# Kernel tuning notes

Measured on AMD Instinct MI355X. Metric: run time of the kernel, lower is better.

Reference implementation:

```python
import jax, jax.numpy as jnp
import numpy as np

# ---- Mamba2 / model hyperparameters (from init_kwargs + mamba_ssm defaults) ----
D_MODEL = 64
D_STATE = 64
D_CONV = 4
EXPAND = 2
HEADDIM = 64                      # mamba_ssm Mamba2 default
D_INNER = EXPAND * D_MODEL        # 128
NHEADS = D_INNER // HEADDIM       # 2
CONV_DIM = D_INNER + 2 * D_STATE  # 256 (ngroups=1)
D_IN_PROJ = 2 * D_INNER + 2 * D_STATE + NHEADS  # 386
B, T, F_ = 4, 128, 128
EPS = 1e-5


def silu(x):
    return x * jax.nn.sigmoid(x)


def depthwise_causal_conv(x, w, b):
    # x: [N, L, C], w: [C, K], b: [C]  (causal depthwise conv, as in Mamba2)
    xt = x.transpose(0, 2, 1)           # [N, C, L]
    kernel = w[:, None, :]              # [C, 1, K]
    y = jax.lax.conv_general_dilated(
        xt, kernel, window_strides=(1,), padding=[(D_CONV - 1, 0)],
        feature_group_count=CONV_DIM)
    return y.transpose(0, 2, 1) + b     # [N, L, C]


def mamba2(u, Wp, cw, cb, dtb, Al, Dp, nw, Wo):
    # u: [N, L, D_MODEL]
    Nb, L, _ = u.shape
    zxbcdt = u @ Wp.T                                   # [N, L, D_IN_PROJ]
    z = zxbcdt[..., :D_INNER]
    xBC = zxbcdt[..., D_INNER:D_INNER + CONV_DIM]
    dt = jax.nn.softplus(zxbcdt[..., -NHEADS:] + dtb)   # [N, L, H]
    xBC = silu(depthwise_causal_conv(xBC, cw, cb))
    x = xBC[..., :D_INNER].reshape(Nb, L, NHEADS, HEADDIM)
    Bm = xBC[..., D_INNER:D_INNER + D_STATE]            # [N, L, Nst]
    Cm = xBC[..., D_INNER + D_STATE:]                   # [N, L, Nst]
    dA = jnp.exp(dt * (-jnp.exp(Al)))                   # [N, L, H]

    def step(h, inp):
        # h: [N, H, P, Nst]
        dA_t, dt_t, x_t, B_t, C_t = inp
        h = h * dA_t[:, :, None, None] + (dt_t[:, :, None] * x_t)[..., None] * B_t[:, None, None, :]
        y = jnp.einsum('bhpn,bn->bhp', h, C_t)
        return h, y

    h0 = jnp.zeros((Nb, NHEADS, HEADDIM, D_STATE), u.dtype)
    xs = (dA.transpose(1, 0, 2), dt.transpose(1, 0, 2),
          x.transpose(1, 0, 2, 3), Bm.transpose(1, 0, 2), Cm.transpose(1, 0, 2))
    _, ys = jax.lax.scan(step, h0, xs)                  # ys: [L, N, H, P]
    y = ys.transpose(1, 0, 2, 3) + Dp[None, None, :, None] * x
    y = y.reshape(Nb, L, D_INNER)
    # RMSNormGated (norm_before_gate=False): gate then rms-normalize
    g = y * silu(z)
    g = g * jax.lax.rsqrt(jnp.mean(g * g, axis=-1, keepdims=True) + EPS) * nw
    return g @ Wo.T                                     # [N, L, D_MODEL]


def bimamba(u, p_fwd, p_bwd, fW, fb):
    out_f = mamba2(u, *p_fwd)
    out_b = mamba2(u[:, ::-1], *p_bwd)[:, ::-1]
    return jnp.concatenate([out_f, out_b], axis=-1) @ fW.T + fb


def layernorm(x, w, b):
    m = jnp.mean(x, axis=-1, keepdims=True)
    v = jnp.mean((x - m) ** 2, axis=-1, keepdims=True)
    return (x - m) * jax.lax.rsqrt(v + EPS) * w + b


def setup_inputs() -> dict:
    key = jax.random.key(0)
    ks = jax.random.split(key, 12)
    inp = {
        'x': jax.random.normal(ks[0], (B, D_MODEL, T, F_), jnp.float32),
        # 4 Mamba2 instances stacked: [freq_fwd, freq_bwd, time_fwd, time_bwd]
        'in_proj_W': 0.02 * jax.random.normal(ks[1], (4, D_IN_PROJ, D_MODEL), jnp.float32),
        'conv_W': 0.1 * jax.random.normal(ks[2], (4, CONV_DIM, D_CONV), jnp.float32),
        'conv_b': jnp.zeros((4, CONV_DIM), jnp.float32),
        'dt_bias': 0.1 * jax.random.normal(ks[3], (4, NHEADS), jnp.float32),
        'A_log': jnp.log(jax.random.uniform(ks[4], (4, NHEADS), jnp.float32, 1.0, 16.0)),
        'D_param': 0.1 * jax.random.normal(ks[5], (4, NHEADS), jnp.float32),
        'norm_w': jnp.ones((4, D_INNER), jnp.float32),
        'out_W': 0.02 * jax.random.normal(ks[6], (4, D_MODEL, D_INNER), jnp.float32),
        # 2 BiMamba fusion linears: [freq, time]
        'fusion_W': 0.02 * jax.random.normal(ks[7], (2, D_MODEL, 2 * D_MODEL), jnp.float32),
        'fusion_b': jnp.zeros((2, D_MODEL), jnp.float32),
        # 2 LayerNorms: [freq, time]
        'ln_w': jnp.ones((2, D_MODEL), jnp.float32),
        'ln_b': jnp.zeros((2, D_MODEL), jnp.float32),
    }
    return inp


def reference(x, in_proj_W, conv_W, conv_b, dt_bias, A_log, D_param, norm_w, out_W,
              fusion_W, fusion_b, ln_w, ln_b):
    Bb, Cc, Tt, Ff = x.shape

    def mp(i):
        return (in_proj_W[i], conv_W[i], conv_b[i], dt_bias[i], A_log[i],
                D_param[i], norm_w[i], out_W[i])

    # ---- frequency axis scan (dilation == 1) ----
    x_freq = x.transpose(0, 2, 3, 1).reshape(Bb * Tt, Ff, Cc)
    xf_out = bimamba(layernorm(x_freq, ln_w[0], ln_b[0]), mp(0), mp(1), fusion_W[0], fusion_b[0])
    x = x + xf_out.reshape(Bb, Tt, Ff, Cc).transpose(0, 3, 1, 2)

    # ---- time axis scan ----
    x_time = x.transpose(0, 3, 2, 1).reshape(Bb * Ff, Tt, Cc)
    xt_out = bimamba(layernorm(x_time, ln_w[1], ln_b[1]), mp(2), mp(3), fusion_W[1], fusion_b[1])
    x = x + xt_out.reshape(Bb, Ff, Tt, Cc).transpose(0, 3, 2, 1)
    return x
```

## Files before the change

### kernel.cpp

```cpp
#include <hip/hip_runtime.h>

#define EPSV 1e-5f

typedef short bf16x8 __attribute__((ext_vector_type(8)));
typedef float f32x4 __attribute__((ext_vector_type(4)));

__device__ __forceinline__ float sigmoidf_(float x) {
  return 1.f / (1.f + __expf(-x));
}
__device__ __forceinline__ unsigned short f2bf(float f) {
  unsigned int u = __float_as_uint(f);
  u += 0x7fffu + ((u >> 16) & 1u);
  return (unsigned short)(u >> 16);
}
__device__ __forceinline__ float bfu(unsigned short h) {
  union { unsigned int u; float f; } t; t.u = ((unsigned int)h) << 16; return t.f;
}
__device__ __forceinline__ float bflo(unsigned int u) {
  union { unsigned int x; float f; } t; t.x = u << 16; return t.f;
}
__device__ __forceinline__ float bfhi(unsigned int u) {
  union { unsigned int x; float f; } t; t.x = u & 0xffff0000u; return t.f;
}

__global__ __launch_bounds__(256) void precomp_wc(
    const float* __restrict__ fW,
    const float* __restrict__ oW,
    float* __restrict__ Wc)
{
  const int bi = blockIdx.x;
  const int i = bi >> 3, mg = bi & 7;
  const int m = (mg << 3) + (threadIdx.x >> 5);
  const int k0 = (threadIdx.x & 31) << 2;
  const int p = i >> 1, d = i & 1;
  const float* fr = fW + p * 8192 + m * 128 + d * 64;
  const float* orow = oW + i * 8192 + k0;
  float a0 = 0.f, a1 = 0.f, a2 = 0.f, a3 = 0.f;
  for (int j = 0; j < 64; ++j) {
    const float f = fr[j];
    const float4 o4 = *(const float4*)(orow + j * 128);
    a0 += f * o4.x; a1 += f * o4.y; a2 += f * o4.z; a3 += f * o4.w;
  }
  float* out = Wc + i * 8192 + m * 128 + k0;
  out[0] = a0; out[1] = a1; out[2] = a2; out[3] = a3;
}

__global__ __launch_bounds__(256) void precomp_wcf(
    const float* __restrict__ Wc, unsigned short* __restrict__ WcF)
{
  const int ip = blockIdx.x;
  const float* src = Wc + (size_t)ip * 8192;
  unsigned short* dst = WcF + (size_t)ip * 8192;
  for (int idx = threadIdx.x; idx < 8192; idx += 256) {
    const int tile = idx >> 11;
    const int h = (idx >> 9) & 3;
    const int lane = (idx >> 3) & 63;
    const int j = idx & 7;
    const int col = lane & 15, quad = lane >> 4;
    dst[idx] = f2bf(src[(tile * 16 + col) * 128 + h * 32 + quad * 8 + j]);
  }
}

__global__ __launch_bounds__(256) void precomp_wpf(
    const float* __restrict__ Wp, unsigned short* __restrict__ WpF)
{
  const int ip = blockIdx.x;
  const float* src = Wp + (size_t)ip * 24704;
  unsigned short* dst = WpF + (size_t)ip * 25600;
  for (int idx = threadIdx.x; idx < 25600; idx += 256) {
    const int tile = idx >> 10;
    const int rem = idx & 1023;
    const int h = rem >> 9;
    const int lane = (rem >> 3) & 63;
    const int j = idx & 7;
    const int col = lane & 15, quad = lane >> 4;
    const int o = tile * 16 + col;
    const int k = h * 32 + quad * 8 + j;
    dst[idx] = (o < 386) ? f2bf(src[o * 64 + k]) : (unsigned short)0;
  }
}

__global__ __launch_bounds__(256) void transp0(
    const float* __restrict__ x, float* __restrict__ x0)
{
  __shared__ float T[64 * 132];
  const int tid = threadIdx.x, blk = blockIdx.x;
  const int b = blk >> 7, t = blk & 127;
  {
    const int c = tid >> 2, f0 = (tid & 3) << 5;
    const float* xp = x + (((size_t)(b * 64 + c) * 128 + t) << 7) + f0;
    float* tp = &T[c * 132 + f0];
    #pragma unroll
    for (int j = 0; j < 8; ++j)
      *(float4*)(tp + (j << 2)) = *(const float4*)(xp + (j << 2));
  }
  __syncthreads();
  {
    const int f = tid >> 1, cb = (tid & 1) << 5;
    float* op = x0 + (((size_t)(b * 128 + t) * 128 + f) << 6) + cb;
    #pragma unroll
    for (int j = 0; j < 32; j += 4) {
      float4 v;
      v.x = T[(cb + j + 0) * 132 + f];
      v.y = T[(cb + j + 1) * 132 + f];
      v.z = T[(cb + j + 2) * 132 + f];
      v.w = T[(cb + j + 3) * 132 + f];
      *(float4*)(op + j) = v;
    }
  }
}

__global__ __launch_bounds__(512, 4) void mamba_dir(
    const float* __restrict__ src,
    unsigned short* __restrict__ ybuf,
    const unsigned short* __restrict__ WpF,
    const unsigned short* __restrict__ WcF,
    const float* __restrict__ cwA, const float* __restrict__ cbA,
    const float* __restrict__ dtbA, const float* __restrict__ AlA,
    const float* __restrict__ DpA, const float* __restrict__ nwA,
    const float* __restrict__ lnwA, const float* __restrict__ lnbA,
    int phase)
{
  __shared__ __align__(16) unsigned short sU[16 * 72];
  __shared__ __align__(16) unsigned short sZb[16 * 136];
  __shared__ __align__(16) float sZx[16 * 260];
  __shared__ __align__(16) unsigned short sBC16[16 * 136];
  __shared__ __align__(16) unsigned short sXdT[128 * 40];
  __shared__ __align__(16) unsigned short sXwT[128 * 40];
  __shared__ __align__(16) unsigned short sBT[64 * 40];
  __shared__ __align__(16) unsigned short sSm[2 * 16 * 40];
  __shared__ __align__(16) unsigned short sH[2 * 64 * 72];
  __shared__ float sMeta[16][2][4];
  __shared__ float sDtRaw[16][2];

  const int tid = threadIdx.x;
  const int blk = blockIdx.x;
  const int seq = blk >> 1, dir = blk & 1;
  const int ip = (phase << 1) + dir;
  const float dtb0 = dtbA[ip * 2], dtb1 = dtbA[ip * 2 + 1];
  const float nA0 = -__expf(AlA[ip * 2]), nA1 = -__expf(AlA[ip * 2 + 1]);
  const float Dp0 = DpA[ip * 2], Dp1 = DpA[ip * 2 + 1];
  const int c256 = tid & 255;
  const int lh = tid >> 8;
  float ch0 = 0.f, ch1 = 0.f, ch2 = 0.f;

  const int wv = tid >> 6, lane = tid & 63;
  const int col = lane & 15, quad = lane >> 4;

  f32x4 hacc[4];
  #pragma unroll
  for (int i = 0; i < 4; ++i) hacc[i] = (f32x4){0.f, 0.f, 0.f, 0.f};

  {
    unsigned int* z;
    z = (unsigned int*)sXdT; for (int i = tid; i < 2560; i += 512) z[i] = 0u;
    z = (unsigned int*)sXwT; for (int i = tid; i < 2560; i += 512) z[i] = 0u;
    z = (unsigned int*)sBT;  for (int i = tid; i < 1280; i += 512) z[i] = 0u;
    z = (unsigned int*)sSm;  for (int i = tid; i < 640;  i += 512) z[i] = 0u;
    z = (unsigned int*)sH;   for (int i = tid; i < 4608; i += 512) z[i] = 0u;
  }

  const unsigned short* wf = WpF + (size_t)ip * 25600;
  const unsigned short* wcf = WcF + (size_t)ip * 8192;
  const size_t sb = (size_t)seq << 13;
  const int pos = tid >> 6, lc = tid & 63;

  float vc0, vc1;
  {
    const int p0 = dir ? (127 - pos) : pos;
    const int p1 = dir ? (127 - (pos + 8)) : (pos + 8);
    vc0 = src[sb + (size_t)p0 * 64 + lc];
    vc1 = src[sb + (size_t)p1 * 64 + lc];
  }

  for (int ck = 0; ck < 8; ++ck) {
    float vn0 = 0.f, vn1 = 0.f;
    if (ck < 7) {
      const int st0 = ((ck + 1) << 4) + pos;
      const int p0 = dir ? (127 - st0) : st0;
      const int p1 = dir ? (127 - (st0 + 8)) : (st0 + 8);
      vn0 = src[sb + (size_t)p0 * 64 + lc];
      vn1 = src[sb + (size_t)p1 * 64 + lc];
    }
    {
      const int lnb_i = (phase << 6) + lc;
      const float lnw_v = lnwA[lnb_i], lnb_v = lnbA[lnb_i];
      #pragma unroll
      for (int half = 0; half < 2; ++half) {
        const float v = half ? vc1 : vc0;
        float sm = v, s2 = v * v;
        sm += __shfl_xor(sm, 1);  s2 += __shfl_xor(s2, 1);
        sm += __shfl_xor(sm, 2);  s2 += __shfl_xor(s2, 2);
        sm += __shfl_xor(sm, 4);  s2 += __shfl_xor(s2, 4);
        sm += __shfl_xor(sm, 8);  s2 += __shfl_xor(s2, 8);
        sm += __shfl_xor(sm, 16); s2 += __shfl_xor(s2, 16);
        sm += __shfl_xor(sm, 32); s2 += __shfl_xor(s2, 32);
        const float mean = sm * (1.f / 64.f);
        const float inv = rsqrtf(s2 * (1.f / 64.f) - mean * mean + EPSV);
        sU[(pos + half * 8) * 72 + lc] = f2bf((v - mean) * inv * lnw_v + lnb_v);
      }
    }
    __syncthreads();
    {
      const bf16x8 a0 = *(const bf16x8*)(&sU[col * 72 + quad * 8]);
      const bf16x8 a1 = *(const bf16x8*)(&sU[col * 72 + quad * 8 + 32]);
      for (int tile = wv; tile < 25; tile += 8) {
        const unsigned short* wt = wf + (tile << 10) + (lane << 3);
        const bf16x8 b0 = *(const bf16x8*)(wt);
        const bf16x8 b1 = *(const bf16x8*)(wt + 512);
        f32x4 d = {0.f, 0.f, 0.f, 0.f};
        d = __builtin_amdgcn_mfma_f32_16x16x32_bf16(a0, b0, d, 0, 0, 0);
        d = __builtin_amdgcn_mfma_f32_16x16x32_bf16(a1, b1, d, 0, 0, 0);
        const int o = (tile << 4) + col;
        if (tile < 8) {
          #pragma unroll
          for (int r = 0; r < 4; ++r)
            sZb[(quad * 4 + r) * 136 + o] = f2bf(d[r]);
        } else if (tile < 24) {
          #pragma unroll
          for (int r = 0; r < 4; ++r)
            sZx[(quad * 4 + r) * 260 + (o - 128)] = d[r];
        } else if (col < 2) {
          #pragma unroll
          for (int r = 0; r < 4; ++r)
            sDtRaw[quad * 4 + r][col] = d[r];
        }
      }
    }
    __syncthreads();
    {
      const int c = c256;
      const float4 cw4 = *(const float4*)(cwA + ip * 1024 + (c << 2));
      const float cbias = cbA[ip * 256 + c];
      float a0c, a1c, a2c;
      if (lh == 0) { a0c = ch0; a1c = ch1; a2c = ch2; }
      else {
        a0c = sZx[5 * 260 + c];
        a1c = sZx[6 * 260 + c];
        a2c = sZx[7 * 260 + c];
      }
      const int lt0 = lh << 3;
      unsigned int pkv[4];
      #pragma unroll
      for (int l = 0; l < 8; ++l) {
        const int lt = lt0 + l;
        const float a3 = sZx[lt * 260 + c];
        const float acc = cbias + a0c * cw4.x + a1c * cw4.y + a2c * cw4.z + a3 * cw4.w;
        const float sv = acc * sigmoidf_(acc);
        const unsigned int hv = (unsigned int)f2bf(sv);
        if (c >= 192)      sBC16[lt * 136 + 64 + (c - 192)] = (unsigned short)hv;
        else if (c >= 128) sBC16[lt * 136 + (c - 128)] = (unsigned short)hv;
        if (l & 1) pkv[l >> 1] |= hv << 16; else pkv[l >> 1] = hv;
        a0c = a1c; a1c = a2c; a2c = a3;
      }
      if (c < 128)
        *(uint4*)(&sXdT[c * 40 + lt0]) = make_uint4(pkv[0], pkv[1], pkv[2], pkv[3]);
      else if (c < 192)
        *(uint4*)(&sBT[(c - 128) * 40 + lt0]) = make_uint4(pkv[0], pkv[1], pkv[2], pkv[3]);
      if (lh == 0) {
        ch0 = sZx[13 * 260 + c];
        ch1 = sZx[14 * 260 + c];
        ch2 = sZx[15 * 260 + c];
      }
      if (tid < 32) {
        const int lt = tid >> 1, hh = tid & 1;
        const float rawv = sDtRaw[lt][hh] + (hh ? dtb1 : dtb0);
        const float dtv = (rawv > 20.f) ? rawv : log1pf(__expf(rawv));
        float Lx = dtv * (hh ? nA1 : nA0);
        #pragma unroll
        for (int d = 2; d < 32; d <<= 1) {
          const float tpv = __shfl_up(Lx, d);
          Lx += (tid >= d) ? tpv : 0.f;
        }
        const float Ltot = __shfl(Lx, 30 + hh);
        *(float4*)(&sMeta[lt][hh][0]) =
            make_float4(Lx, dtv, __expf(Ltot - Lx) * dtv, __expf(Lx));
      }
    }
    __syncthreads();
    if (wv == 0) {
      const bf16x8 ca0 = *(const bf16x8*)(&sBC16[col * 136 + 64 + quad * 8]);
      const bf16x8 ca1 = *(const bf16x8*)(&sBC16[col * 136 + 96 + quad * 8]);
      const bf16x8 bb0 = *(const bf16x8*)(&sBC16[col * 136 + quad * 8]);
      const bf16x8 bb1 = *(const bf16x8*)(&sBC16[col * 136 + 32 + quad * 8]);
      f32x4 g = {0.f, 0.f, 0.f, 0.f};
      g = __builtin_amdgcn_mfma_f32_16x16x32_bf16(ca0, bb0, g, 0, 0, 0);
      g = __builtin_amdgcn_mfma_f32_16x16x32_bf16(ca1, bb1, g, 0, 0, 0);
      #pragma unroll
      for (int h = 0; h < 2; ++h) {
        const float Ls = sMeta[col][h][0];
        const float dts = sMeta[col][h][1];
        #pragma unroll
        for (int r = 0; r < 4; ++r) {
          const int t = quad * 4 + r;
          const float m = (col <= t) ? __expf(sMeta[t][h][0] - Ls) * dts : 0.f;
          sSm[(h * 16 + t) * 40 + col] = f2bf(g[r] * m);
        }
      }
    } else if (wv <= 2) {
      if (ck < 7) {
        const int p = ((wv - 1) << 6) + lane;
        const int hh = p >> 6;
        #pragma unroll
        for (int tp = 0; tp < 8; ++tp) {
          const unsigned int xr = *(const unsigned int*)(&sXdT[p * 40 + tp * 2]);
          const unsigned int lo = (unsigned int)f2bf(bflo(xr) * sMeta[tp * 2][hh][2]);
          const unsigned int hi = (unsigned int)f2bf(bfhi(xr) * sMeta[tp * 2 + 1][hh][2]);
          *(unsigned int*)(&sXwT[p * 40 + tp * 2]) = lo | (hi << 16);
        }
      }
    } else if (wv >= 4) {
      const int h = (wv - 4) >> 1, pt2 = (wv - 4) & 1;
      const int cb0 = h * 64 + pt2 * 32;
      if (ck) {
        const bf16x8 ca0 = *(const bf16x8*)(&sBC16[col * 136 + 64 + quad * 8]);
        const bf16x8 ca1 = *(const bf16x8*)(&sBC16[col * 136 + 96 + quad * 8]);
        #pragma unroll
        for (int half = 0; half < 2; ++half) {
          const unsigned short* hp = &sH[(cb0 + half * 16 + col) * 72];
          const bf16x8 h0 = *(const bf16x8*)(hp + quad * 8);
          const bf16x8 h1 = *(const bf16x8*)(hp + 32 + quad * 8);
          f32x4 d = {0.f, 0.f, 0.f, 0.f};
          d = __builtin_amdgcn_mfma_f32_16x16x32_bf16(ca0, h0, d, 0, 0, 0);
          d = __builtin_amdgcn_mfma_f32_16x16x32_bf16(ca1, h1, d, 0, 0, 0);
          #pragma unroll
          for (int r = 0; r < 4; ++r)
            sZx[(quad * 4 + r) * 260 + cb0 + half * 16 + col] =
                d[r] * sMeta[quad * 4 + r][h][3];
        }
      } else {
        #pragma unroll
        for (int r = 0; r < 4; ++r) {
          sZx[(quad * 4 + r) * 260 + cb0 + col] = 0.f;
          sZx[(quad * 4 + r) * 260 + cb0 + 16 + col] = 0.f;
        }
      }
    }
    __syncthreads();
    if (ck < 7) {
      const int h = wv >> 2;
      const int pb = wv << 4;
      const float At = sMeta[15][h][3];
      const bf16x8 xa = *(const bf16x8*)(&sXwT[(pb + col) * 40 + quad * 8]);
      #pragma unroll
      for (int nt = 0; nt < 4; ++nt) {
        const bf16x8 bbt = *(const bf16x8*)(&sBT[(nt * 16 + col) * 40 + quad * 8]);
        #pragma unroll
        for (int r = 0; r < 4; ++r) hacc[nt][r] *= At;
        hacc[nt] = __builtin_amdgcn_mfma_f32_16x16x32_bf16(xa, bbt, hacc[nt], 0, 0, 0);
      }
      #pragma unroll
      for (int nt = 0; nt < 4; ++nt) {
        #pragma unroll
        for (int r = 0; r < 4; ++r)
          sH[(pb + quad * 4 + r) * 72 + nt * 16 + col] = f2bf(hacc[nt][r]);
      }
    }
    __syncthreads();
    {
      const int h = wv >> 2;
      const int c = (wv << 4) + col;
      const float dp = h ? Dp1 : Dp0;
      const bf16x8 sa = *(const bf16x8*)(&sSm[(h * 16 + col) * 40 + quad * 8]);
      const bf16x8 xb = *(const bf16x8*)(&sXdT[c * 40 + quad * 8]);
      f32x4 cin;
      #pragma unroll
      for (int r = 0; r < 4; ++r) cin[r] = sZx[(quad * 4 + r) * 260 + c];
      f32x4 yD = __builtin_amdgcn_mfma_f32_16x16x32_bf16(sa, xb, cin, 0, 0, 0);
      const uint2 xw = *(const uint2*)(&sXdT[c * 40 + quad * 4]);
      yD[0] += dp * bflo(xw.x); yD[1] += dp * bfhi(xw.x);
      yD[2] += dp * bflo(xw.y); yD[3] += dp * bfhi(xw.y);
      #pragma unroll
      for (int r = 0; r < 4; ++r)
        sZx[(quad * 4 + r) * 260 + c] = yD[r];
    }
    __syncthreads();
    {
      const int k0 = lc << 1;
      const float2 nw2 = *(const float2*)(nwA + ip * 128 + k0);
      #pragma unroll
      for (int sub = 0; sub < 2; ++sub) {
        const int lt = wv + (sub << 3);
        const float2 yv = *(const float2*)(&sZx[lt * 260 + k0]);
        const unsigned int zp = *(const unsigned int*)(&sZb[lt * 136 + k0]);
        const float z0 = bflo(zp), z1 = bfhi(zp);
        const float g0 = yv.x * (z0 * sigmoidf_(z0));
        const float g1 = yv.y * (z1 * sigmoidf_(z1));
        float ssq = g0 * g0 + g1 * g1;
        ssq += __shfl_xor(ssq, 1);
        ssq += __shfl_xor(ssq, 2);
        ssq += __shfl_xor(ssq, 4);
        ssq += __shfl_xor(ssq, 8);
        ssq += __shfl_xor(ssq, 16);
        ssq += __shfl_xor(ssq, 32);
        const float sc = rsqrtf(ssq * (1.f / 128.f) + EPSV);
        const unsigned int lo = f2bf(g0 * sc * nw2.x);
        const unsigned int hi = f2bf(g1 * sc * nw2.y);
        *(unsigned int*)(&sZb[lt * 136 + k0]) = lo | (hi << 16);
      }
    }
    __syncthreads();
    {
      if (wv < 4) {
        const unsigned short* wt = wcf + (wv << 11);
        f32x4 d = {0.f, 0.f, 0.f, 0.f};
        #pragma unroll
        for (int h = 0; h < 4; ++h) {
          const bf16x8 a = *(const bf16x8*)(&sZb[col * 136 + (h << 5) + (quad << 3)]);
          const bf16x8 bb = *(const bf16x8*)(wt + (h << 9) + (lane << 3));
          d = __builtin_amdgcn_mfma_f32_16x16x32_bf16(a, bb, d, 0, 0, 0);
        }
        const size_t yb = ((size_t)(dir * 512 + seq) * 128) << 6;
        #pragma unroll
        for (int r = 0; r < 4; ++r) {
          const int pp = (quad << 2) + r;
          const int st = (ck << 4) + pp, rp = dir ? (127 - st) : st;
          ybuf[yb + ((size_t)rp << 6) + (wv << 4) + col] = f2bf(d[r]);
        }
      }
    }
    vc0 = vn0; vc1 = vn1;
  }
}

__global__ __launch_bounds__(256) void combine0(
    const float* __restrict__ x, const unsigned short* __restrict__ ybuf,
    const float* __restrict__ fb, float* __restrict__ x1)
{
  __shared__ float T[64 * 132];
  const int tid = threadIdx.x, blk = blockIdx.x;
  const int b = blk >> 7, t = blk & 127;
  {
    const int c = tid >> 2, f0 = (tid & 3) << 5;
    const float* xp = x + (((size_t)(b * 64 + c) * 128 + t) << 7) + f0;
    float* tp = &T[c * 132 + f0];
    #pragma unroll
    for (int j = 0; j < 8; ++j)
      *(float4*)(tp + (j << 2)) = *(const float4*)(xp + (j << 2));
  }
  __syncthreads();
  {
    const int f = tid >> 1, cb = (tid & 1) << 5;
    const size_t s0 = (size_t)b * 128 + t;
    const unsigned short* yf = ybuf + ((s0 * 128 + f) << 6) + cb;
    const unsigned short* yb = ybuf + (((s0 + 512) * 128 + f) << 6) + cb;
    float* op = x1 + (((size_t)(b * 128 + f) * 128 + t) << 6) + cb;
    #pragma unroll
    for (int j = 0; j < 32; j += 4) {
      float4 v;
      v.x = T[(cb + j + 0) * 132 + f] + bfu(yf[j + 0]) + bfu(yb[j + 0]) + fb[cb + j + 0];
      v.y = T[(cb + j + 1) * 132 + f] + bfu(yf[j + 1]) + bfu(yb[j + 1]) + fb[cb + j + 1];
      v.z = T[(cb + j + 2) * 132 + f] + bfu(yf[j + 2]) + bfu(yb[j + 2]) + fb[cb + j + 2];
      v.w = T[(cb + j + 3) * 132 + f] + bfu(yf[j + 3]) + bfu(yb[j + 3]) + fb[cb + j + 3];
      *(float4*)(op + j) = v;
    }
  }
}

__global__ __launch_bounds__(256) void combine1(
    const float* __restrict__ x1, const unsigned short* __restrict__ ybuf,
    const float* __restrict__ fb, float* __restrict__ out)
{
  __shared__ float T[128 * 68];
  const int tid = threadIdx.x, blk = blockIdx.x;
  const int b = blk >> 7, t = blk & 127;
  {
    const int f = tid >> 1, cb = (tid & 1) << 5;
    const size_t s1 = (size_t)b * 128 + f;
    const float* xp = x1 + ((s1 * 128 + t) << 6) + cb;
    const unsigned short* yf = ybuf + ((s1 * 128 + t) << 6) + cb;
    const unsigned short* yb = ybuf + (((s1 + 512) * 128 + t) << 6) + cb;
    float* tp = &T[f * 68 + cb];
    #pragma unroll
    for (int j = 0; j < 32; j += 4) {
      const float4 xv = *(const float4*)(xp + j);
      const uint2 yfv = *(const uint2*)(yf + j);
      const uint2 ybv = *(const uint2*)(yb + j);
      const float4 fv = *(const float4*)(fb + cb + j);
      tp[j + 0] = xv.x + bflo(yfv.x) + bflo(ybv.x) + fv.x;
      tp[j + 1] = xv.y + bfhi(yfv.x) + bfhi(ybv.x) + fv.y;
      tp[j + 2] = xv.z + bflo(yfv.y) + bflo(ybv.y) + fv.z;
      tp[j + 3] = xv.w + bfhi(yfv.y) + bfhi(ybv.y) + fv.w;
    }
  }
  __syncthreads();
  {
    const int c = tid >> 2, f0 = (tid & 3) << 5;
    float* op = out + (((size_t)(b * 64 + c) * 128 + t) << 7) + f0;
    #pragma unroll
    for (int j = 0; j < 32; j += 4) {
      float4 v;
      v.x = T[(f0 + j + 0) * 68 + c];
      v.y = T[(f0 + j + 1) * 68 + c];
      v.z = T[(f0 + j + 2) * 68 + c];
      v.w = T[(f0 + j + 3) * 68 + c];
      *(float4*)(op + j) = v;
    }
  }
}

extern "C" void kernel_launch(void* const* d_in, const int* in_sizes, int n_in,
                              void* d_out, int out_size, void* d_ws, size_t ws_size,
                              hipStream_t stream) {
  const float* x   = (const float*)d_in[0];
  const float* Wp  = (const float*)d_in[1];
  const float* cw  = (const float*)d_in[2];
  const float* cb  = (const float*)d_in[3];
  const float* dtb = (const float*)d_in[4];
  const float* Al  = (const float*)d_in[5];
  const float* Dp  = (const float*)d_in[6];
  const float* nw  = (const float*)d_in[7];
  const float* oW  = (const float*)d_in[8];
  const float* fW  = (const float*)d_in[9];
  const float* fb  = (const float*)d_in[10];
  const float* lnw = (const float*)d_in[11];
  const float* lnb = (const float*)d_in[12];

  float* ws = (float*)d_ws;
  float* Wc = ws;
  unsigned short* WpF = (unsigned short*)(ws + 32768);
  unsigned short* WcF = (unsigned short*)(ws + 32768 + 51200);
  float* xbuf = ws + 32768 + 51200 + 16384;
  unsigned short* y = (unsigned short*)(xbuf + 4194304);

  precomp_wc<<<32, 256, 0, stream>>>(fW, oW, Wc);
  precomp_wcf<<<4, 256, 0, stream>>>(Wc, WcF);
  precomp_wpf<<<4, 256, 0, stream>>>(Wp, WpF);
  transp0<<<512, 256, 0, stream>>>(x, xbuf);
  mamba_dir<<<1024, 512, 0, stream>>>(xbuf, y, WpF, WcF, cw, cb, dtb, Al, Dp,
                                      nw, lnw, lnb, 0);
  combine0<<<512, 256, 0, stream>>>(x, y, fb, xbuf);
  mamba_dir<<<1024, 512, 0, stream>>>(xbuf, y, WpF, WcF, cw, cb, dtb, Al, Dp,
                                      nw, lnw, lnb, 1);
  combine1<<<512, 256, 0, stream>>>(xbuf, y, fb + 64, (float*)d_out);
}
```

Before: 382.2 us.

## Overlap next-chunk LayerNorm with out-projection on idle waves

The LayerNorm of the next 16-row chunk now runs on waves 4-7 while waves 0-3 do the output-projection MFMA, instead of all waves doing it at the start of each chunk. The first chunk is normalized before the loop, and the loads for the next chunk are issued early. This takes the LayerNorm step and one barrier off the critical path, at the cost of an extra barrier at the end of each iteration and more work on half the waves.

```diff
diff --git a/kernel.cpp b/kernel.cpp
--- a/kernel.cpp
+++ b/kernel.cpp
@@ -21,6 +21,20 @@
 }
 __device__ __forceinline__ float bfhi(unsigned int u) {
   union { unsigned int x; float f; } t; t.x = u & 0xffff0000u; return t.f;
+}
+__device__ __forceinline__ void ln_row(float v, int row, int lane,
+                                       float lnw_v, float lnb_v,
+                                       unsigned short* sU) {
+  float sm = v, s2 = v * v;
+  sm += __shfl_xor(sm, 1);  s2 += __shfl_xor(s2, 1);
+  sm += __shfl_xor(sm, 2);  s2 += __shfl_xor(s2, 2);
+  sm += __shfl_xor(sm, 4);  s2 += __shfl_xor(s2, 4);
+  sm += __shfl_xor(sm, 8);  s2 += __shfl_xor(s2, 8);
+  sm += __shfl_xor(sm, 16); s2 += __shfl_xor(s2, 16);
+  sm += __shfl_xor(sm, 32); s2 += __shfl_xor(s2, 32);
+  const float mean = sm * (1.f / 64.f);
+  const float inv = rsqrtf(s2 * (1.f / 64.f) - mean * mean + EPSV);
+  sU[row * 72 + lane] = f2bf((v - mean) * inv * lnw_v + lnb_v);
 }
 
 __global__ __launch_bounds__(256) void precomp_wc(
@@ -163,44 +177,33 @@
   const unsigned short* wf = WpF + (size_t)ip * 25600;
   const unsigned short* wcf = WcF + (size_t)ip * 8192;
   const size_t sb = (size_t)seq << 13;
-  const int pos = tid >> 6, lc = tid & 63;
-
-  float vc0, vc1;
-  {
-    const int p0 = dir ? (127 - pos) : pos;
-    const int p1 = dir ? (127 - (pos + 8)) : (pos + 8);
-    vc0 = src[sb + (size_t)p0 * 64 + lc];
-    vc1 = src[sb + (size_t)p1 * 64 + lc];
-  }
+
+  if (wv >= 4) {
+    float v0[4];
+    #pragma unroll
+    for (int h = 0; h < 4; ++h) {
+      const int lr = ((wv - 4) << 2) + h;
+      const int p = dir ? (127 - lr) : lr;
+      v0[h] = src[sb + (size_t)p * 64 + lane];
+    }
+    const int lnb_i = (phase << 6) + lane;
+    const float lnw_v = lnwA[lnb_i], lnb_v = lnbA[lnb_i];
+    #pragma unroll
+    for (int h = 0; h < 4; ++h)
+      ln_row(v0[h], ((wv - 4) << 2) + h, lane, lnw_v, lnb_v, sU);
+  }
+  __syncthreads();
 
   for (int ck = 0; ck < 8; ++ck) {
-    float vn0 = 0.f, vn1 = 0.f;
-    if (ck < 7) {
-      const int st0 = ((ck + 1) << 4) + pos;
-      const int p0 = dir ? (127 - st0) : st0;
-      const int p1 = dir ? (127 - (st0 + 8)) : (st0 + 8);
-      vn0 = src[sb + (size_t)p0 * 64 + lc];
-      vn1 = src[sb + (size_t)p1 * 64 + lc];
-    }
-    {
-      const int lnb_i = (phase << 6) + lc;
-      const float lnw_v = lnwA[lnb_i], lnb_v = lnbA[lnb_i];
-      #pragma unroll
-      for (int half = 0; half < 2; ++half) {
-        const float v = half ? vc1 : vc0;
-        float sm = v, s2 = v * v;
-        sm += __shfl_xor(sm, 1);  s2 += __shfl_xor(s2, 1);
-        sm += __shfl_xor(sm, 2);  s2 += __shfl_xor(s2, 2);
-        sm += __shfl_xor(sm, 4);  s2 += __shfl_xor(s2, 4);
-        sm += __shfl_xor(sm, 8);  s2 += __shfl_xor(s2, 8);
-        sm += __shfl_xor(sm, 16); s2 += __shfl_xor(s2, 16);
-        sm += __shfl_xor(sm, 32); s2 += __shfl_xor(s2, 32);
-        const float mean = sm * (1.f / 64.f);
-        const float inv = rsqrtf(s2 * (1.f / 64.f) - mean * mean + EPSV);
-        sU[(pos + half * 8) * 72 + lc] = f2bf((v - mean) * inv * lnw_v + lnb_v);
-      }
-    }
-    __syncthreads();
+    float v4[4] = {0.f, 0.f, 0.f, 0.f};
+    if (wv >= 4 && ck < 7) {
+      #pragma unroll
+      for (int h = 0; h < 4; ++h) {
+        const int st = ((ck + 1) << 4) + ((wv - 4) << 2) + h;
+        const int p = dir ? (127 - st) : st;
+        v4[h] = src[sb + (size_t)p * 64 + lane];
+      }
+    }
     {
       const bf16x8 a0 = *(const bf16x8*)(&sU[col * 72 + quad * 8]);
       const bf16x8 a1 = *(const bf16x8*)(&sU[col * 72 + quad * 8 + 32]);
@@ -376,7 +379,7 @@
     }
     __syncthreads();
     {
-      const int k0 = lc << 1;
+      const int k0 = lane << 1;
       const float2 nw2 = *(const float2*)(nwA + ip * 128 + k0);
       #pragma unroll
       for (int sub = 0; sub < 2; ++sub) {
@@ -400,26 +403,30 @@
       }
     }
     __syncthreads();
-    {
-      if (wv < 4) {
-        const unsigned short* wt = wcf + (wv << 11);
-        f32x4 d = {0.f, 0.f, 0.f, 0.f};
-        #pragma unroll
-        for (int h = 0; h < 4; ++h) {
-          const bf16x8 a = *(const bf16x8*)(&sZb[col * 136 + (h << 5) + (quad << 3)]);
-          const bf16x8 bb = *(const bf16x8*)(wt + (h << 9) + (lane << 3));
-          d = __builtin_amdgcn_mfma_f32_16x16x32_bf16(a, bb, d, 0, 0, 0);
-        }
-        const size_t yb = ((size_t)(dir * 512 + seq) * 128) << 6;
-        #pragma unroll
-        for (int r = 0; r < 4; ++r) {
-          const int pp = (quad << 2) + r;
-          const int st = (ck << 4) + pp, rp = dir ? (127 - st) : st;
-          ybuf[yb + ((size_t)rp << 6) + (wv << 4) + col] = f2bf(d[r]);
-        }
-      }
-    }
-    vc0 = vn0; vc1 = vn1;
+    if (wv < 4) {
+      const unsigned short* wt = wcf + (wv << 11);
+      f32x4 d = {0.f, 0.f, 0.f, 0.f};
+      #pragma unroll
+      for (int h = 0; h < 4; ++h) {
+        const bf16x8 a = *(const bf16x8*)(&sZb[col * 136 + (h << 5) + (quad << 3)]);
+        const bf16x8 bb = *(const bf16x8*)(wt + (h << 9) + (lane << 3));
+        d = __builtin_amdgcn_mfma_f32_16x16x32_bf16(a, bb, d, 0, 0, 0);
+      }
+      const size_t yb = ((size_t)(dir * 512 + seq) * 128) << 6;
+      #pragma unroll
+      for (int r = 0; r < 4; ++r) {
+        const int pp = (quad << 2) + r;
+        const int st = (ck << 4) + pp, rp = dir ? (127 - st) : st;
+        ybuf[yb + ((size_t)rp << 6) + (wv << 4) + col] = f2bf(d[r]);
+      }
+    } else if (ck < 7) {
+      const int lnb_i = (phase << 6) + lane;
+      const float lnw_v = lnwA[lnb_i], lnb_v = lnbA[lnb_i];
+      #pragma unroll
+      for (int h = 0; h < 4; ++h)
+        ln_row(v4[h], ((wv - 4) << 2) + h, lane, lnw_v, lnb_v, sU);
+    }
+    __syncthreads();
   }
 }
 
```

Result: slower. 390.8 us (+2.2%).
